# Performance work log

Hardware: AMD Instinct MI355X
Metric: run time of the kernel (lower is better)

## Reference

```python
import jax, jax.numpy as jnp
import numpy as np

D_MODEL = 4096
N_HEADS = 32
N_KV_HEADS = 8
HEAD_DIM = D_MODEL // N_HEADS  # 128
SEQ = 2048
BATCH = 1
ROPE_BASE = 10000.0


def build_rope_cache(max_seq_len, head_dim, base=10000.0):
    half = head_dim // 2
    pos = jnp.arange(max_seq_len, dtype=jnp.float32)
    inv_freqs = 1.0 / (base ** (jnp.arange(half, dtype=jnp.float32) / half))
    angles = pos[:, None] * inv_freqs[None, :]  # (S, half)
    return jnp.cos(angles), jnp.sin(angles)


def apply_rope(t, cos, sin):
    # t: (B, H, S, D); cos/sin: (S, D//2) broadcast over batch & heads.
    t_even = t[..., 0::2]
    t_odd = t[..., 1::2]
    c = cos[None, None, :, :]
    s = sin[None, None, :, :]
    rot_even = t_even * c - t_odd * s
    rot_odd = t_even * s + t_odd * c
    # interleave back into even/odd slots
    return jnp.stack([rot_even, rot_odd], axis=-1).reshape(t.shape)


def setup_inputs() -> dict:
    key = jax.random.key(0)
    kx, kq, kk, kv, ko = jax.random.split(key, 5)
    bound = 1.0 / np.sqrt(D_MODEL)
    x = jax.random.normal(kx, (BATCH, SEQ, D_MODEL), dtype=jnp.float32)
    # torch Linear weights: (out_features, in_features)
    wq = jax.random.uniform(kq, (N_HEADS * HEAD_DIM, D_MODEL), minval=-bound, maxval=bound, dtype=jnp.float32)
    wk = jax.random.uniform(kk, (N_KV_HEADS * HEAD_DIM, D_MODEL), minval=-bound, maxval=bound, dtype=jnp.float32)
    wv = jax.random.uniform(kv, (N_KV_HEADS * HEAD_DIM, D_MODEL), minval=-bound, maxval=bound, dtype=jnp.float32)
    wo = jax.random.uniform(ko, (D_MODEL, D_MODEL), minval=-bound, maxval=bound, dtype=jnp.float32)
    attn_mask = jnp.tril(jnp.ones((SEQ, SEQ), dtype=jnp.int32))[None, None, :, :]
    return {"x": x, "wq": wq, "wk": wk, "wv": wv, "wo": wo, "attn_mask": attn_mask}


def reference(x, wq, wk, wv, wo, attn_mask):
    B, S, _ = x.shape
    cos, sin = build_rope_cache(SEQ, HEAD_DIM, ROPE_BASE)
    cos, sin = cos[:S], sin[:S]
    q = (x @ wq.T).reshape(B, S, N_HEADS, HEAD_DIM).transpose(0, 2, 1, 3)      # (B,H,S,D)
    k = (x @ wk.T).reshape(B, S, N_KV_HEADS, HEAD_DIM).transpose(0, 2, 1, 3)   # (B,Hkv,S,D)
    v = (x @ wv.T).reshape(B, S, N_KV_HEADS, HEAD_DIM).transpose(0, 2, 1, 3)
    q = apply_rope(q, cos, sin)
    k = apply_rope(k, cos, sin)
    n_rep = N_HEADS // N_KV_HEADS
    if n_rep > 1:
        k = jnp.repeat(k, n_rep, axis=1)
        v = jnp.repeat(v, n_rep, axis=1)
    scores = jnp.einsum('bhqd,bhkd->bhqk', q, k) / jnp.sqrt(jnp.float32(HEAD_DIM))
    scores = jnp.where(attn_mask == 0, -jnp.inf, scores)
    attn = jax.nn.softmax(scores, axis=-1)
    out = jnp.einsum('bhqk,bhkd->bhqd', attn, v)
    out = out.transpose(0, 2, 1, 3).reshape(B, S, D_MODEL)
    return out @ wo.T
```

## Files before the change

### kernel.cpp

```cpp
#include <hip/hip_runtime.h>
#include <hip/hip_bf16.h>

typedef float f32x2 __attribute__((ext_vector_type(2)));
typedef float f32x4 __attribute__((ext_vector_type(4)));
typedef __bf16 bf16x4 __attribute__((ext_vector_type(4)));
typedef __bf16 bf16x8 __attribute__((ext_vector_type(8)));

__device__ __forceinline__ void gld_lds16(const void* g, void* l) {
  __builtin_amdgcn_global_load_lds((const __attribute__((address_space(1))) void*)g,
                                   (__attribute__((address_space(3))) void*)l, 16, 0, 0);
}

__global__ void cvt_f32_bf16(const float* __restrict__ in, __bf16* __restrict__ out,
                             int n8) {
  int idx = blockIdx.x * blockDim.x + threadIdx.x;
  if (idx >= n8) return;
  f32x4 a = *(const f32x4*)(in + (size_t)idx * 8);
  f32x4 b = *(const f32x4*)(in + (size_t)idx * 8 + 4);
  bf16x8 o;
#pragma unroll
  for (int j = 0; j < 4; ++j) { o[j] = (__bf16)a[j]; o[4 + j] = (__bf16)b[j]; }
  *(bf16x8*)(out + (size_t)idx * 8) = o;
}

__global__ void cvt_f32_bf16_2(const float* __restrict__ inA,
                               const float* __restrict__ inB,
                               __bf16* __restrict__ out, int n8half) {
  int idx = blockIdx.x * blockDim.x + threadIdx.x;
  if (idx >= 2 * n8half) return;
  const float* src = (idx < n8half) ? inA + (size_t)idx * 8
                                    : inB + (size_t)(idx - n8half) * 8;
  f32x4 a = *(const f32x4*)src;
  f32x4 b = *(const f32x4*)(src + 4);
  bf16x8 o;
#pragma unroll
  for (int j = 0; j < 4; ++j) { o[j] = (__bf16)a[j]; o[4 + j] = (__bf16)b[j]; }
  *(bf16x8*)(out + (size_t)idx * 8) = o;
}

__global__ void build_trig(float* __restrict__ trig) {
  int idx = blockIdx.x * blockDim.x + threadIdx.x;
  if (idx >= 2048 * 64) return;
  int i = idx & 63, s = idx >> 6;
  float ang = (float)s * powf(10000.0f, -(float)i * (1.0f / 64.0f));
  float sn, cs;
  sincosf(ang, &sn, &cs);
  trig[idx * 2] = cs;
  trig[idx * 2 + 1] = sn;
}

template <int BM, int BN, typename OutT, bool KVF>
__global__ __launch_bounds__(256) void gemm_bf16(const __bf16* __restrict__ A,
                                                 const __bf16* __restrict__ B0,
                                                 const __bf16* __restrict__ B1,
                                                 int Nsplit, OutT* __restrict__ C,
                                                 int M, int N, int K,
                                                 const float* __restrict__ trig,
                                                 __bf16* __restrict__ Vt) {
  constexpr int MI = BM / 32, NJ = BN / 32;
  constexpr int RA = BM / 32, RB = BN / 32;
  __shared__ __bf16 As[BM * 64] __attribute__((aligned(16)));
  __shared__ __bf16 Bs[BN * 64] __attribute__((aligned(16)));

  const int tid = threadIdx.x;
  const int lane = tid & 63;
  const int w = tid >> 6;
  const int nwg = gridDim.x * gridDim.y;
  const int orig = blockIdx.y * gridDim.x + blockIdx.x;
  const int wgid = (orig & 7) * (nwg >> 3) + (orig >> 3);
  const int m0 = (wgid % gridDim.x) * BM;
  const int n0 = (wgid / gridDim.x) * BN;
  const int li = lane & 15, lg = lane >> 4;

  const __bf16* bsrc[RB];
#pragma unroll
  for (int i = 0; i < RB; ++i) {
    int slot = i * 256 + w * 64 + lane;
    int row = slot >> 3;
    int sch = (slot & 7) ^ (row & 7);
    int n = n0 + row;
    bsrc[i] = (n < Nsplit ? B0 + (size_t)n * K : B1 + (size_t)(n - Nsplit) * K) +
              sch * 8;
  }
  const __bf16* asrc[RA];
#pragma unroll
  for (int i = 0; i < RA; ++i) {
    int slot = i * 256 + w * 64 + lane;
    int row = slot >> 3;
    int sch = (slot & 7) ^ (row & 7);
    asrc[i] = A + (size_t)(m0 + row) * K + sch * 8;
  }

  const int wr = (w >> 1) * (BM / 2);
  const int wc = (w & 1) * (BN / 2);

  f32x4 acc[MI][NJ] = {};

  for (int k0 = 0; k0 < K; k0 += 64) {
    __syncthreads();
#pragma unroll
    for (int i = 0; i < RA; ++i)
      gld_lds16(asrc[i] + k0, &As[(i * 256 + w * 64) * 8]);
#pragma unroll
    for (int i = 0; i < RB; ++i)
      gld_lds16(bsrc[i] + k0, &Bs[(i * 256 + w * 64) * 8]);
    __syncthreads();

#pragma unroll
    for (int u = 0; u < 2; ++u) {
      bf16x8 af[MI], bfr[NJ];
#pragma unroll
      for (int mi = 0; mi < MI; ++mi)
        af[mi] = *(const bf16x8*)&As[(wr + mi * 16 + li) * 64 +
                                     (((u * 4 + lg) ^ (li & 7)) * 8)];
#pragma unroll
      for (int nj = 0; nj < NJ; ++nj)
        bfr[nj] = *(const bf16x8*)&Bs[(wc + nj * 16 + li) * 64 +
                                      (((u * 4 + lg) ^ (li & 7)) * 8)];
#pragma unroll
      for (int mi = 0; mi < MI; ++mi)
#pragma unroll
        for (int nj = 0; nj < NJ; ++nj)
          acc[mi][nj] = __builtin_amdgcn_mfma_f32_16x16x32_bf16(af[mi], bfr[nj],
                                                                acc[mi][nj], 0, 0, 0);
    }
  }

  const int crow = lg * 4;
  if (KVF && n0 >= Nsplit) {
#pragma unroll
    for (int mi = 0; mi < MI; ++mi)
#pragma unroll
      for (int nj = 0; nj < NJ; ++nj) {
        int d = n0 - Nsplit + wc + nj * 16 + li;
        int sb = m0 + wr + mi * 16 + crow;
        bf16x4 pk;
#pragma unroll
        for (int r = 0; r < 4; ++r) pk[r] = (__bf16)acc[mi][nj][r];
        *(bf16x4*)&Vt[(size_t)d * 2048 + sb] = pk;
      }
  } else if (KVF) {
#pragma unroll
    for (int mi = 0; mi < MI; ++mi)
#pragma unroll
      for (int nj = 0; nj < NJ; ++nj) {
        int c = n0 + wc + nj * 16 + li;
        int i = (c & 127) >> 1;
        bool even = (c & 1) == 0;
#pragma unroll
        for (int r = 0; r < 4; ++r) {
          int s = m0 + wr + mi * 16 + crow + r;
          float own = acc[mi][nj][r];
          float oth = __shfl_xor(own, 1);
          f32x2 cs = *(const f32x2*)&trig[((size_t)s * 64 + i) * 2];
          float v = even ? (own * cs[0] - oth * cs[1])
                         : (oth * cs[1] + own * cs[0]);
          C[(size_t)s * N + c] = (OutT)v;
        }
      }
  } else {
#pragma unroll
    for (int mi = 0; mi < MI; ++mi)
#pragma unroll
      for (int nj = 0; nj < NJ; ++nj)
#pragma unroll
        for (int r = 0; r < 4; ++r)
          C[(size_t)(m0 + wr + mi * 16 + crow + r) * N + (n0 + wc + nj * 16 + li)] =
              (OutT)acc[mi][nj][r];
  }
}

__global__ __launch_bounds__(256) void attn_fwd_v8(const __bf16* __restrict__ Q,
                                                   const __bf16* __restrict__ KVb,
                                                   const __bf16* __restrict__ Vt,
                                                   const float* __restrict__ trig,
                                                   __bf16* __restrict__ O) {
  const int tid = threadIdx.x;
  const int lane = tid & 63;
  const int w = tid >> 6;
  const int bid = blockIdx.x;
  const int xcd = bid & 7;
  const int r9 = bid >> 3;
  const int h = xcd * 4 + (r9 & 3);
  const int mb = 31 - (r9 >> 2);
  const int kvh = h >> 2;
  const int m0 = mb * 64;
  const int rbase = m0 + w * 16;

  __shared__ __bf16 Ks[3][32 * 128] __attribute__((aligned(16)));
  __shared__ __bf16 Vs[3][128 * 32] __attribute__((aligned(16)));
  __shared__ __bf16 Ps[4][16 * 40] __attribute__((aligned(16)));

  const int li = lane & 15, lg = lane >> 4;
  const float qscale = 0.08838834764831845f * 1.4426950408889634f;

  auto stage_k = [&](int k0, int buf) {
#pragma unroll
    for (int i = 0; i < 2; ++i) {
      int slot = i * 256 + tid;
      int row = slot >> 4;
      int sch = (slot & 15) ^ (row & 7);
      gld_lds16(&KVb[(size_t)(k0 + row) * 2048 + kvh * 128 + sch * 8],
                &Ks[buf][(i * 256 + w * 64) * 8]);
    }
  };
  auto stage_v = [&](int k0, int buf) {
#pragma unroll
    for (int i = 0; i < 2; ++i) {
      int slot = i * 256 + tid;
      int row = slot >> 2;
      int sch = (slot & 3) ^ (row & 3);
      gld_lds16(&Vt[(size_t)(kvh * 128 + row) * 2048 + k0 + sch * 8],
                &Vs[buf][(i * 256 + w * 64) * 8]);
    }
  };

  const int s = rbase + li;
  bf16x8 qf[4];
  {
    const __bf16* qrow = Q + (size_t)s * 4096 + h * 128;
#pragma unroll
    for (int kc = 0; kc < 4; ++kc) {
      bf16x8 raw = *(const bf16x8*)(qrow + kc * 32 + lg * 8);
#pragma unroll
      for (int jj = 0; jj < 4; ++jj) {
        int i = kc * 16 + lg * 4 + jj;
        f32x2 cs = *(const f32x2*)&trig[((size_t)s * 64 + i) * 2];
        float e = (float)raw[2 * jj], o = (float)raw[2 * jj + 1];
        qf[kc][2 * jj]     = (__bf16)((e * cs[0] - o * cs[1]) * qscale);
        qf[kc][2 * jj + 1] = (__bf16)((e * cs[1] + o * cs[0]) * qscale);
      }
    }
  }

  f32x4 accO[8] = {};
  float plane = 0.f;
  const int ntile = 2 * (mb + 1);

  stage_v(0, 0);
  stage_k(0, 0);

#pragma unroll 1
  for (int t = 0; t < ntile; ++t) {
    const int k0 = t * 32;
    const int cb = t % 3;
    const int nk = (t + 1 < ntile) ? k0 + 32 : k0;
    stage_v(nk, (t + 1) % 3);
    stage_k(nk, (t + 1) % 3);

    asm volatile("s_waitcnt vmcnt(4)" ::: "memory");
    __builtin_amdgcn_s_barrier();
    __builtin_amdgcn_sched_barrier(0);

    f32x4 s2[2] = {};
    __builtin_amdgcn_s_setprio(1);
#pragma unroll
    for (int nt = 0; nt < 2; ++nt)
#pragma unroll
      for (int kc = 0; kc < 4; ++kc) {
        bf16x8 kf = *(const bf16x8*)&Ks[cb][(li + 16 * nt) * 128 +
                                           (((4 * kc + lg) ^ (li & 7)) * 8)];
        s2[nt] = __builtin_amdgcn_mfma_f32_16x16x32_bf16(kf, qf[kc], s2[nt], 0, 0, 0);
      }
    __builtin_amdgcn_s_setprio(0);

    const bool needmask = (k0 + 31 > rbase);
#pragma unroll
    for (int nt = 0; nt < 2; ++nt) {
      bf16x4 pk;
#pragma unroll
      for (int rr = 0; rr < 4; ++rr) {
        const int key = k0 + 16 * nt + lg * 4 + rr;
        float v = s2[nt][rr];
        if (needmask && key > s) v = -INFINITY;
        float p = exp2f(v);
        plane += p;
        pk[rr] = (__bf16)p;
      }
      *(bf16x4*)&Ps[w][li * 40 + 16 * nt + lg * 4] = pk;
    }
    bf16x8 pa = *(const bf16x8*)&Ps[w][li * 40 + lg * 8];

    __builtin_amdgcn_s_setprio(1);
#pragma unroll
    for (int dt = 0; dt < 8; ++dt) {
      bf16x8 vf = *(const bf16x8*)&Vs[cb][(li + 16 * dt) * 32 +
                                          ((lg ^ (li & 3)) * 8)];
      accO[dt] = __builtin_amdgcn_mfma_f32_16x16x32_bf16(pa, vf, accO[dt], 0, 0, 0);
    }
    __builtin_amdgcn_s_setprio(0);
  }

  {
    float sum = plane;
    sum += __shfl_xor(sum, 16);
    sum += __shfl_xor(sum, 32);
    float inv[4];
#pragma unroll
    for (int rr = 0; rr < 4; ++rr) inv[rr] = 1.0f / __shfl(sum, lg * 4 + rr);
#pragma unroll
    for (int dt = 0; dt < 8; ++dt)
#pragma unroll
      for (int rr = 0; rr < 4; ++rr)
        O[(size_t)(rbase + lg * 4 + rr) * 4096 + h * 128 + dt * 16 + li] =
            (__bf16)(accO[dt][rr] * inv[rr]);
  }
}

extern "C" void kernel_launch(void* const* d_in, const int* in_sizes, int n_in,
                              void* d_out, int out_size, void* d_ws, size_t ws_size,
                              hipStream_t stream) {
  const float* x  = (const float*)d_in[0];
  const float* wq = (const float*)d_in[1];
  const float* wk = (const float*)d_in[2];
  const float* wv = (const float*)d_in[3];
  const float* wo = (const float*)d_in[4];
  float* out = (float*)d_out;

  const int S = 2048, D = 4096;
  char* ws = (char*)d_ws;
  __bf16* xb  = (__bf16*)ws;
  __bf16* Qb  = (__bf16*)(ws + 16777216);
  __bf16* KVb = (__bf16*)(ws + 33554432);
  __bf16* Vt  = (__bf16*)(ws + 41943040);
  __bf16* wb  = (__bf16*)(ws + 46137344);
  float*  trig = (float*)(ws + 79691776);
  __bf16* AOb = xb;

  cvt_f32_bf16<<<(S * D / 8 + 255) / 256, 256, 0, stream>>>(x, xb, S * D / 8);
  cvt_f32_bf16<<<(D * D / 8 + 255) / 256, 256, 0, stream>>>(wq, wb, D * D / 8);
  gemm_bf16<128, 128, __bf16, false><<<dim3(16, 32), 256, 0, stream>>>(
      xb, wb, wb, 1 << 30, Qb, S, D, D, nullptr, nullptr);

  build_trig<<<(2048 * 64 + 255) / 256, 256, 0, stream>>>(trig);

  cvt_f32_bf16_2<<<(2 * 1024 * D / 8 + 255) / 256, 256, 0, stream>>>(
      wk, wv, wb, 1024 * D / 8);
  gemm_bf16<64, 128, __bf16, true><<<dim3(32, 16), 256, 0, stream>>>(
      xb, wb, wb + (size_t)1024 * D, 1024, KVb, S, 2048, D, trig, Vt);

  attn_fwd_v8<<<1024, 256, 0, stream>>>(Qb, KVb, Vt, trig, AOb);

  cvt_f32_bf16<<<(D * D / 8 + 255) / 256, 256, 0, stream>>>(wo, wb, D * D / 8);
  gemm_bf16<128, 128, float, false><<<dim3(16, 32), 256, 0, stream>>>(
      AOb, wb, wb, 1 << 30, out, S, D, D, nullptr, nullptr);
}
```

Before: 345.5 us.

## Double attention query tile per block and fold weight conversions into neighbors

The attention kernel now gives each wave two 16-row query tiles, so a block covers 128 rows. Each staged K/V tile is reused for twice as many MFMAs, and the grid halves to 512 blocks. The wo fp32-to-bf16 conversion moves into the tail of the lighter-loaded attention blocks (mb<=11), and the RoPE trig table is built inside the x-conversion kernel, removing two launches. The trade-offs are higher register pressure from doubled accumulators and a coarser causal load balance across fewer, larger blocks.

```diff
diff --git a/kernel.cpp b/kernel.cpp
--- a/kernel.cpp
+++ b/kernel.cpp
@@ -38,15 +38,25 @@
   *(bf16x8*)(out + (size_t)idx * 8) = o;
 }
 
-__global__ void build_trig(float* __restrict__ trig) {
+__global__ void cvt_x_trig(const float* __restrict__ in, __bf16* __restrict__ out,
+                           int n8, float* __restrict__ trig, int ntrig) {
   int idx = blockIdx.x * blockDim.x + threadIdx.x;
-  if (idx >= 2048 * 64) return;
-  int i = idx & 63, s = idx >> 6;
-  float ang = (float)s * powf(10000.0f, -(float)i * (1.0f / 64.0f));
-  float sn, cs;
-  sincosf(ang, &sn, &cs);
-  trig[idx * 2] = cs;
-  trig[idx * 2 + 1] = sn;
+  if (idx < n8) {
+    f32x4 a = *(const f32x4*)(in + (size_t)idx * 8);
+    f32x4 b = *(const f32x4*)(in + (size_t)idx * 8 + 4);
+    bf16x8 o;
+#pragma unroll
+    for (int j = 0; j < 4; ++j) { o[j] = (__bf16)a[j]; o[4 + j] = (__bf16)b[j]; }
+    *(bf16x8*)(out + (size_t)idx * 8) = o;
+  } else if (idx - n8 < ntrig) {
+    int t = idx - n8;
+    int i = t & 63, s = t >> 6;
+    float ang = (float)s * powf(10000.0f, -(float)i * (1.0f / 64.0f));
+    float sn, cs;
+    sincosf(ang, &sn, &cs);
+    trig[t * 2] = cs;
+    trig[t * 2 + 1] = sn;
+  }
 }
 
 template <int BM, int BN, typename OutT, bool KVF>
@@ -170,11 +180,13 @@
   }
 }
 
-__global__ __launch_bounds__(256) void attn_fwd_v8(const __bf16* __restrict__ Q,
+__global__ __launch_bounds__(256) void attn_fwd_v9(const __bf16* __restrict__ Q,
                                                    const __bf16* __restrict__ KVb,
                                                    const __bf16* __restrict__ Vt,
                                                    const float* __restrict__ trig,
-                                                   __bf16* __restrict__ O) {
+                                                   __bf16* __restrict__ O,
+                                                   const float* __restrict__ wo,
+                                                   __bf16* __restrict__ wob) {
   const int tid = threadIdx.x;
   const int lane = tid & 63;
   const int w = tid >> 6;
@@ -182,14 +194,14 @@
   const int xcd = bid & 7;
   const int r9 = bid >> 3;
   const int h = xcd * 4 + (r9 & 3);
-  const int mb = 31 - (r9 >> 2);
+  const int mb = 15 - (r9 >> 2);
   const int kvh = h >> 2;
-  const int m0 = mb * 64;
-  const int rbase = m0 + w * 16;
+  const int m0 = mb * 128;
+  const int rbase = m0 + w * 32;
 
   __shared__ __bf16 Ks[3][32 * 128] __attribute__((aligned(16)));
   __shared__ __bf16 Vs[3][128 * 32] __attribute__((aligned(16)));
-  __shared__ __bf16 Ps[4][16 * 40] __attribute__((aligned(16)));
+  __shared__ __bf16 Ps[4][32 * 40] __attribute__((aligned(16)));
 
   const int li = lane & 15, lg = lane >> 4;
   const float qscale = 0.08838834764831845f * 1.4426950408889634f;
@@ -215,9 +227,10 @@
     }
   };
 
-  const int s = rbase + li;
-  bf16x8 qf[4];
-  {
+  bf16x8 qf[2][4];
+#pragma unroll
+  for (int mt = 0; mt < 2; ++mt) {
+    const int s = rbase + mt * 16 + li;
     const __bf16* qrow = Q + (size_t)s * 4096 + h * 128;
 #pragma unroll
     for (int kc = 0; kc < 4; ++kc) {
@@ -227,15 +240,15 @@
         int i = kc * 16 + lg * 4 + jj;
         f32x2 cs = *(const f32x2*)&trig[((size_t)s * 64 + i) * 2];
         float e = (float)raw[2 * jj], o = (float)raw[2 * jj + 1];
-        qf[kc][2 * jj]     = (__bf16)((e * cs[0] - o * cs[1]) * qscale);
-        qf[kc][2 * jj + 1] = (__bf16)((e * cs[1] + o * cs[0]) * qscale);
-      }
-    }
-  }
-
-  f32x4 accO[8] = {};
-  float plane = 0.f;
-  const int ntile = 2 * (mb + 1);
+        qf[mt][kc][2 * jj]     = (__bf16)((e * cs[0] - o * cs[1]) * qscale);
+        qf[mt][kc][2 * jj + 1] = (__bf16)((e * cs[1] + o * cs[0]) * qscale);
+      }
+    }
+  }
+
+  f32x4 accO[2][8] = {};
+  float plane[2] = {0.f, 0.f};
+  const int ntile = (m0 + 128) >> 5;
 
   stage_v(0, 0);
   stage_k(0, 0);
@@ -252,7 +265,7 @@
     __builtin_amdgcn_s_barrier();
     __builtin_amdgcn_sched_barrier(0);
 
-    f32x4 s2[2] = {};
+    f32x4 s2[2][2] = {};
     __builtin_amdgcn_s_setprio(1);
 #pragma unroll
     for (int nt = 0; nt < 2; ++nt)
@@ -260,39 +273,47 @@
       for (int kc = 0; kc < 4; ++kc) {
         bf16x8 kf = *(const bf16x8*)&Ks[cb][(li + 16 * nt) * 128 +
                                            (((4 * kc + lg) ^ (li & 7)) * 8)];
-        s2[nt] = __builtin_amdgcn_mfma_f32_16x16x32_bf16(kf, qf[kc], s2[nt], 0, 0, 0);
+        s2[nt][0] = __builtin_amdgcn_mfma_f32_16x16x32_bf16(kf, qf[0][kc], s2[nt][0], 0, 0, 0);
+        s2[nt][1] = __builtin_amdgcn_mfma_f32_16x16x32_bf16(kf, qf[1][kc], s2[nt][1], 0, 0, 0);
       }
     __builtin_amdgcn_s_setprio(0);
 
-    const bool needmask = (k0 + 31 > rbase);
-#pragma unroll
-    for (int nt = 0; nt < 2; ++nt) {
-      bf16x4 pk;
-#pragma unroll
-      for (int rr = 0; rr < 4; ++rr) {
-        const int key = k0 + 16 * nt + lg * 4 + rr;
-        float v = s2[nt][rr];
-        if (needmask && key > s) v = -INFINITY;
-        float p = exp2f(v);
-        plane += p;
-        pk[rr] = (__bf16)p;
-      }
-      *(bf16x4*)&Ps[w][li * 40 + 16 * nt + lg * 4] = pk;
-    }
-    bf16x8 pa = *(const bf16x8*)&Ps[w][li * 40 + lg * 8];
+    bf16x8 pa[2];
+#pragma unroll
+    for (int mt = 0; mt < 2; ++mt) {
+      const int s = rbase + mt * 16 + li;
+      const bool needmask = (k0 + 31 > rbase + mt * 16);
+#pragma unroll
+      for (int nt = 0; nt < 2; ++nt) {
+        bf16x4 pk;
+#pragma unroll
+        for (int rr = 0; rr < 4; ++rr) {
+          const int key = k0 + 16 * nt + lg * 4 + rr;
+          float v = s2[nt][mt][rr];
+          if (needmask && key > s) v = -INFINITY;
+          float p = exp2f(v);
+          plane[mt] += p;
+          pk[rr] = (__bf16)p;
+        }
+        *(bf16x4*)&Ps[w][(mt * 16 + li) * 40 + 16 * nt + lg * 4] = pk;
+      }
+      pa[mt] = *(const bf16x8*)&Ps[w][(mt * 16 + li) * 40 + lg * 8];
+    }
 
     __builtin_amdgcn_s_setprio(1);
 #pragma unroll
     for (int dt = 0; dt < 8; ++dt) {
       bf16x8 vf = *(const bf16x8*)&Vs[cb][(li + 16 * dt) * 32 +
                                           ((lg ^ (li & 3)) * 8)];
-      accO[dt] = __builtin_amdgcn_mfma_f32_16x16x32_bf16(pa, vf, accO[dt], 0, 0, 0);
+      accO[0][dt] = __builtin_amdgcn_mfma_f32_16x16x32_bf16(pa[0], vf, accO[0][dt], 0, 0, 0);
+      accO[1][dt] = __builtin_amdgcn_mfma_f32_16x16x32_bf16(pa[1], vf, accO[1][dt], 0, 0, 0);
     }
     __builtin_amdgcn_s_setprio(0);
   }
 
-  {
-    float sum = plane;
+#pragma unroll
+  for (int mt = 0; mt < 2; ++mt) {
+    float sum = plane[mt];
     sum += __shfl_xor(sum, 16);
     sum += __shfl_xor(sum, 32);
     float inv[4];
@@ -302,8 +323,21 @@
     for (int dt = 0; dt < 8; ++dt)
 #pragma unroll
       for (int rr = 0; rr < 4; ++rr)
-        O[(size_t)(rbase + lg * 4 + rr) * 4096 + h * 128 + dt * 16 + li] =
-            (__bf16)(accO[dt][rr] * inv[rr]);
+        O[(size_t)(rbase + mt * 16 + lg * 4 + rr) * 4096 + h * 128 + dt * 16 + li] =
+            (__bf16)(accO[mt][dt][rr] * inv[rr]);
+  }
+
+  if (mb <= 11) {
+    const int u = (11 - mb) + 12 * ((r9 & 3) + 4 * xcd);
+    const int n8 = 4096 * 4096 / 8;
+    for (int idx = u * 256 + tid; idx < n8; idx += 384 * 256) {
+      f32x4 a = *(const f32x4*)(wo + (size_t)idx * 8);
+      f32x4 b = *(const f32x4*)(wo + (size_t)idx * 8 + 4);
+      bf16x8 o;
+#pragma unroll
+      for (int j = 0; j < 4; ++j) { o[j] = (__bf16)a[j]; o[4 + j] = (__bf16)b[j]; }
+      *(bf16x8*)(wob + (size_t)idx * 8) = o;
+    }
   }
 }
 
@@ -327,21 +361,20 @@
   float*  trig = (float*)(ws + 79691776);
   __bf16* AOb = xb;
 
-  cvt_f32_bf16<<<(S * D / 8 + 255) / 256, 256, 0, stream>>>(x, xb, S * D / 8);
+  cvt_x_trig<<<(S * D / 8 + 2048 * 64 + 255) / 256, 256, 0, stream>>>(
+      x, xb, S * D / 8, trig, 2048 * 64);
+
   cvt_f32_bf16<<<(D * D / 8 + 255) / 256, 256, 0, stream>>>(wq, wb, D * D / 8);
   gemm_bf16<128, 128, __bf16, false><<<dim3(16, 32), 256, 0, stream>>>(
       xb, wb, wb, 1 << 30, Qb, S, D, D, nullptr, nullptr);
-
-  build_trig<<<(2048 * 64 + 255) / 256, 256, 0, stream>>>(trig);
 
   cvt_f32_bf16_2<<<(2 * 1024 * D / 8 + 255) / 256, 256, 0, stream>>>(
       wk, wv, wb, 1024 * D / 8);
   gemm_bf16<64, 128, __bf16, true><<<dim3(32, 16), 256, 0, stream>>>(
       xb, wb, wb + (size_t)1024 * D, 1024, KVb, S, 2048, D, trig, Vt);
 
-  attn_fwd_v8<<<1024, 256, 0, stream>>>(Qb, KVb, Vt, trig, AOb);
-
-  cvt_f32_bf16<<<(D * D / 8 + 255) / 256, 256, 0, stream>>>(wo, wb, D * D / 8);
+  attn_fwd_v9<<<512, 256, 0, stream>>>(Qb, KVb, Vt, trig, AOb, wo, wb);
+
   gemm_bf16<128, 128, float, false><<<dim3(16, 32), 256, 0, stream>>>(
       AOb, wb, wb, 1 << 30, out, S, D, D, nullptr, nullptr);
 }
```

New measurement: 344.3 us. No clear change (-0.4%).

## Fuse trig table into x conversion and wo conversion into attention tail

Applied to the files above, without the earlier changes.

The RoPE trig table build is merged into the x fp32→bf16 conversion kernel, which removes one launch. The wo fp32→bf16 conversion now runs at the end of the attention kernel, split across the 768 blocks with lower query-block indices. Under the causal mask those blocks have less attention work, so the memory-bound weight conversion can overlap with the heavier blocks still computing and fill otherwise idle CUs. The cost is extra register and code pressure in the attention kernel, and the conversion work is now tied to attention block scheduling.

```diff
diff --git a/kernel.cpp b/kernel.cpp
--- a/kernel.cpp
+++ b/kernel.cpp
@@ -38,15 +38,25 @@
   *(bf16x8*)(out + (size_t)idx * 8) = o;
 }
 
-__global__ void build_trig(float* __restrict__ trig) {
+__global__ void cvt_x_trig(const float* __restrict__ in, __bf16* __restrict__ out,
+                           int n8, float* __restrict__ trig, int ntrig) {
   int idx = blockIdx.x * blockDim.x + threadIdx.x;
-  if (idx >= 2048 * 64) return;
-  int i = idx & 63, s = idx >> 6;
-  float ang = (float)s * powf(10000.0f, -(float)i * (1.0f / 64.0f));
-  float sn, cs;
-  sincosf(ang, &sn, &cs);
-  trig[idx * 2] = cs;
-  trig[idx * 2 + 1] = sn;
+  if (idx < n8) {
+    f32x4 a = *(const f32x4*)(in + (size_t)idx * 8);
+    f32x4 b = *(const f32x4*)(in + (size_t)idx * 8 + 4);
+    bf16x8 o;
+#pragma unroll
+    for (int j = 0; j < 4; ++j) { o[j] = (__bf16)a[j]; o[4 + j] = (__bf16)b[j]; }
+    *(bf16x8*)(out + (size_t)idx * 8) = o;
+  } else if (idx - n8 < ntrig) {
+    int t = idx - n8;
+    int i = t & 63, s = t >> 6;
+    float ang = (float)s * powf(10000.0f, -(float)i * (1.0f / 64.0f));
+    float sn, cs;
+    sincosf(ang, &sn, &cs);
+    trig[t * 2] = cs;
+    trig[t * 2 + 1] = sn;
+  }
 }
 
 template <int BM, int BN, typename OutT, bool KVF>
@@ -170,11 +180,13 @@
   }
 }
 
-__global__ __launch_bounds__(256) void attn_fwd_v8(const __bf16* __restrict__ Q,
-                                                   const __bf16* __restrict__ KVb,
-                                                   const __bf16* __restrict__ Vt,
-                                                   const float* __restrict__ trig,
-                                                   __bf16* __restrict__ O) {
+__global__ __launch_bounds__(256) void attn_fwd_v8f(const __bf16* __restrict__ Q,
+                                                    const __bf16* __restrict__ KVb,
+                                                    const __bf16* __restrict__ Vt,
+                                                    const float* __restrict__ trig,
+                                                    __bf16* __restrict__ O,
+                                                    const float* __restrict__ wo,
+                                                    __bf16* __restrict__ wob) {
   const int tid = threadIdx.x;
   const int lane = tid & 63;
   const int w = tid >> 6;
@@ -305,6 +317,19 @@
         O[(size_t)(rbase + lg * 4 + rr) * 4096 + h * 128 + dt * 16 + li] =
             (__bf16)(accO[dt][rr] * inv[rr]);
   }
+
+  if (mb <= 23) {
+    const int u = (23 - mb) + 24 * ((r9 & 3) + 4 * xcd);
+    const int n8 = 4096 * 4096 / 8;
+    for (int idx = u * 256 + tid; idx < n8; idx += 768 * 256) {
+      f32x4 a = *(const f32x4*)(wo + (size_t)idx * 8);
+      f32x4 b = *(const f32x4*)(wo + (size_t)idx * 8 + 4);
+      bf16x8 o;
+#pragma unroll
+      for (int j = 0; j < 4; ++j) { o[j] = (__bf16)a[j]; o[4 + j] = (__bf16)b[j]; }
+      *(bf16x8*)(wob + (size_t)idx * 8) = o;
+    }
+  }
 }
 
 extern "C" void kernel_launch(void* const* d_in, const int* in_sizes, int n_in,
@@ -327,21 +352,20 @@
   float*  trig = (float*)(ws + 79691776);
   __bf16* AOb = xb;
 
-  cvt_f32_bf16<<<(S * D / 8 + 255) / 256, 256, 0, stream>>>(x, xb, S * D / 8);
+  cvt_x_trig<<<(S * D / 8 + 2048 * 64 + 255) / 256, 256, 0, stream>>>(
+      x, xb, S * D / 8, trig, 2048 * 64);
+
   cvt_f32_bf16<<<(D * D / 8 + 255) / 256, 256, 0, stream>>>(wq, wb, D * D / 8);
   gemm_bf16<128, 128, __bf16, false><<<dim3(16, 32), 256, 0, stream>>>(
       xb, wb, wb, 1 << 30, Qb, S, D, D, nullptr, nullptr);
-
-  build_trig<<<(2048 * 64 + 255) / 256, 256, 0, stream>>>(trig);
 
   cvt_f32_bf16_2<<<(2 * 1024 * D / 8 + 255) / 256, 256, 0, stream>>>(
       wk, wv, wb, 1024 * D / 8);
   gemm_bf16<64, 128, __bf16, true><<<dim3(32, 16), 256, 0, stream>>>(
       xb, wb, wb + (size_t)1024 * D, 1024, KVb, S, 2048, D, trig, Vt);
 
-  attn_fwd_v8<<<1024, 256, 0, stream>>>(Qb, KVb, Vt, trig, AOb);
-
-  cvt_f32_bf16<<<(D * D / 8 + 255) / 256, 256, 0, stream>>>(wo, wb, D * D / 8);
+  attn_fwd_v8f<<<1024, 256, 0, stream>>>(Qb, KVb, Vt, trig, AOb, wo, wb);
+
   gemm_bf16<128, 128, float, false><<<dim3(16, 32), 256, 0, stream>>>(
       AOb, wb, wb, 1 << 30, out, S, D, D, nullptr, nullptr);
 }
```

Result: no change. 344.1 us (-0.4%).
